# Kernel tuning notes

Hardware: AMD Instinct MI355X
Metric: run time of the kernel (lower is better)

## Reference

```python
import jax, jax.numpy as jnp
import numpy as np

NBINS = 256  # skimage threshold_otsu default
RGB_W = jnp.array([0.2989, 0.5870, 0.1140], dtype=jnp.float32)  # tf.image.rgb_to_grayscale weights


def threshold_otsu(img):
    """Global Otsu threshold over all pixels, matching skimage.filters.threshold_otsu."""
    vmin = img.min()
    vmax = img.max()
    edges = jnp.linspace(vmin, vmax, NBINS + 1)
    centers = (edges[:-1] + edges[1:]) * 0.5
    hist = jnp.histogram(img.ravel(), bins=edges)[0].astype(jnp.float32)
    # class probabilities / cumulative weights
    w1 = jnp.cumsum(hist)                      # weight of class <= t
    w2 = jnp.cumsum(hist[::-1])[::-1]          # weight of class > t
    hc = hist * centers
    s1 = jnp.cumsum(hc)
    s2 = jnp.cumsum(hc[::-1])[::-1]
    m1 = s1 / jnp.maximum(w1, 1.0)
    m2 = s2 / jnp.maximum(w2, 1.0)
    # inter-class variance at each split point
    var12 = w1[:-1] * w2[1:] * (m1[:-1] - m2[1:]) ** 2
    idx = jnp.argmax(var12)
    return centers[idx]


def setup_inputs() -> dict:
    key = jax.random.key(0)
    inputs = jax.random.uniform(key, (32, 128, 2048, 3), dtype=jnp.float32)
    return {"inputs": inputs}


def reference(inputs) -> jnp.ndarray:
    # rgb_to_grayscale on first 3 channels, keep channel dim -> [B,H,W,1]
    gray = jnp.einsum('bhwc,c->bhw', inputs[..., :3].astype(jnp.float32), RGB_W)[..., None]
    thresh = threshold_otsu(gray)
    binarized = (gray > thresh).astype(jnp.float32)   # [B,H,W,1]
    # channels == 3 -> tile grayscale binarization back to 3 channels
    binarized = jnp.tile(binarized, (1, 1, 1, 3))
    return binarized
```

## Files before the change

### kernel.cpp

```cpp
#include <hip/hip_runtime.h>

static constexpr int HIST_OFF   = 2;
static constexpr int EDGES_OFF  = 258;
static constexpr int VMIN_OFF   = 515;
static constexpr int DELTA_OFF  = 516;
static constexpr int INVD_OFF   = 517;
static constexpr int THRESH_OFF = 518;
static constexpr size_t GRAY_BYTE_OFF = 4096;

typedef float nfloat4 __attribute__((ext_vector_type(4)));

#define GLOAD_LDS16(gp, lp)                                                    \
    __builtin_amdgcn_global_load_lds(                                          \
        (const __attribute__((address_space(1))) void*)(gp),                   \
        (__attribute__((address_space(3))) void*)(lp), 16, 0, 0)

__device__ __forceinline__ unsigned fkey(float x) {
    unsigned u = __float_as_uint(x);
    return (u & 0x80000000u) ? ~u : (u | 0x80000000u);
}
__device__ __forceinline__ float keyf(unsigned k) {
    return (k & 0x80000000u) ? __uint_as_float(k & 0x7FFFFFFFu)
                             : __uint_as_float(~k);
}
__device__ __forceinline__ float gray1(float r, float g, float b) {
    float t0 = __fmul_rn(r, 0.2989f);
    float t1 = __fmul_rn(g, 0.5870f);
    float t2 = __fmul_rn(b, 0.1140f);
    return __fadd_rn(__fadd_rn(t0, t1), t2);
}

__global__ void init_kernel(unsigned* __restrict__ wsu) {
    int i = threadIdx.x;
    if (i < 256) wsu[HIST_OFF + i] = 0u;
    if (i == 0) { wsu[0] = 0xFFFFFFFFu; wsu[1] = 0u; }
}

__global__ void __launch_bounds__(256)
gray_minmax_async(const float* __restrict__ in, float* __restrict__ gray,
                  unsigned* __restrict__ wsu, int npix4) {
    __shared__ float4 sbuf[4][2][192];
    __shared__ unsigned smn[4], smx[4];
    const float4* in4 = (const float4*)in;
    float4* gray4 = (float4*)gray;
    const int lane = threadIdx.x & 63;
    const int w = threadIdx.x >> 6;
    const int gw = blockIdx.x * 4 + w;
    const size_t wbase4 = (size_t)gw * 768;
    unsigned mn = 0xFFFFFFFFu, mx = 0u;

#pragma unroll
    for (int k = 0; k < 3; ++k)
        GLOAD_LDS16(in4 + wbase4 + 64 * k + lane, &sbuf[w][0][64 * k]);

#pragma unroll
    for (int t = 0; t < 4; ++t) {
        const int cb = t & 1;
        if (t < 3) {
#pragma unroll
            for (int k = 0; k < 3; ++k)
                GLOAD_LDS16(in4 + wbase4 + (size_t)(t + 1) * 192 + 64 * k + lane,
                            &sbuf[w][cb ^ 1][64 * k]);
            __builtin_amdgcn_s_waitcnt(0x0F73);
        } else {
            __builtin_amdgcn_s_waitcnt(0x0F71);
        }
        float4 c0 = sbuf[w][cb][3 * lane + 0];
        float4 c1 = sbuf[w][cb][3 * lane + 1];
        float4 c2 = sbuf[w][cb][3 * lane + 2];
        float g0 = gray1(c0.x, c0.y, c0.z);
        float g1 = gray1(c0.w, c1.x, c1.y);
        float g2 = gray1(c1.z, c1.w, c2.x);
        float g3 = gray1(c2.y, c2.z, c2.w);
        gray4[(size_t)gw * 256 + t * 64 + lane] = make_float4(g0, g1, g2, g3);
        unsigned k0 = fkey(g0), k1 = fkey(g1), k2 = fkey(g2), k3 = fkey(g3);
        mn = min(mn, min(min(k0, k1), min(k2, k3)));
        mx = max(mx, max(max(k0, k1), max(k2, k3)));
    }
    for (int off = 32; off > 0; off >>= 1) {
        mn = min(mn, (unsigned)__shfl_xor((int)mn, off, 64));
        mx = max(mx, (unsigned)__shfl_xor((int)mx, off, 64));
    }
    if (lane == 0) { smn[w] = mn; smx[w] = mx; }
    __syncthreads();
    if (threadIdx.x == 0) {
        mn = min(min(smn[0], smn[1]), min(smn[2], smn[3]));
        mx = max(max(smx[0], smx[1]), max(smx[2], smx[3]));
        atomicMin(&wsu[0], mn);
        atomicMax(&wsu[1], mx);
    }
}

__global__ void __launch_bounds__(256)
gray_minmax_generic(const float* __restrict__ in, float* __restrict__ gray,
                    unsigned* __restrict__ wsu, int npix4) {
    __shared__ unsigned smn[4], smx[4];
    const float4* in4 = (const float4*)in;
    const int stride = gridDim.x * blockDim.x;
    unsigned mn = 0xFFFFFFFFu, mx = 0u;
    for (int t = blockIdx.x * blockDim.x + threadIdx.x; t < npix4; t += stride) {
        const float4* p = in4 + (size_t)t * 3;
        float4 c0 = p[0], c1 = p[1], c2 = p[2];
        float g0 = gray1(c0.x, c0.y, c0.z);
        float g1 = gray1(c0.w, c1.x, c1.y);
        float g2 = gray1(c1.z, c1.w, c2.x);
        float g3 = gray1(c2.y, c2.z, c2.w);
        if (gray) ((float4*)gray)[t] = make_float4(g0, g1, g2, g3);
        unsigned k0 = fkey(g0), k1 = fkey(g1), k2 = fkey(g2), k3 = fkey(g3);
        mn = min(mn, min(min(k0, k1), min(k2, k3)));
        mx = max(mx, max(max(k0, k1), max(k2, k3)));
    }
    for (int off = 32; off > 0; off >>= 1) {
        mn = min(mn, (unsigned)__shfl_xor((int)mn, off, 64));
        mx = max(mx, (unsigned)__shfl_xor((int)mx, off, 64));
    }
    int wave = threadIdx.x >> 6;
    if ((threadIdx.x & 63) == 0) { smn[wave] = mn; smx[wave] = mx; }
    __syncthreads();
    if (threadIdx.x == 0) {
        mn = min(min(smn[0], smn[1]), min(smn[2], smn[3]));
        mx = max(max(smx[0], smx[1]), max(smx[2], smx[3]));
        atomicMin(&wsu[0], mn);
        atomicMax(&wsu[1], mx);
    }
}

__global__ void edges_kernel(const unsigned* __restrict__ wsu,
                             float* __restrict__ wsf) {
    float vmin = keyf(wsu[0]);
    float vmax = keyf(wsu[1]);
    float delta = __fdiv_rn(__fsub_rn(vmax, vmin), 256.0f);
    int i = threadIdx.x;
    if (i <= 256) {
        float e = (i == 256) ? vmax
                             : __fadd_rn(vmin, __fmul_rn((float)i, delta));
        wsf[EDGES_OFF + i] = e;
    }
    if (i == 0) {
        wsf[VMIN_OFF]  = vmin;
        wsf[DELTA_OFF] = delta;
        wsf[INVD_OFF]  = (delta > 0.0f) ? __fdiv_rn(1.0f, delta) : 0.0f;
    }
}

__device__ __forceinline__ void bin4(float x0, float x1, float x2, float x3,
                                     const float* eds, float vmin, float invd,
                                     unsigned* lh) {
    float xs[4] = {x0, x1, x2, x3};
#pragma unroll
    for (int j = 0; j < 4; ++j) {
        float x = xs[j];
        int b = (int)(__fmul_rn(__fsub_rn(x, vmin), invd));
        b = b < 0 ? 0 : (b > 255 ? 255 : b);
        while (b < 255 && x >= eds[b + 1]) ++b;
        while (b > 0 && x < eds[b]) --b;
        atomicAdd(&lh[b], 1u);
    }
}

__global__ void __launch_bounds__(256)
hist_kernel(const float* __restrict__ gray, const float* __restrict__ in,
            const float* __restrict__ wsf, unsigned* __restrict__ wsu,
            int npix4) {
    __shared__ float eds[257];
    __shared__ unsigned lh[256];
    for (int i = threadIdx.x; i < 257; i += blockDim.x)
        eds[i] = wsf[EDGES_OFF + i];
    if (threadIdx.x < 256) lh[threadIdx.x] = 0u;
    __syncthreads();
    const float vmin = eds[0];
    const float invd = wsf[INVD_OFF];
    const int stride = gridDim.x * blockDim.x;
    const int base = blockIdx.x * blockDim.x + threadIdx.x;
    if (gray && base + 7 * stride < npix4) {
        float4 g[8];
#pragma unroll
        for (int j = 0; j < 8; ++j) g[j] = ((const float4*)gray)[base + j * stride];
#pragma unroll
        for (int j = 0; j < 8; ++j)
            bin4(g[j].x, g[j].y, g[j].z, g[j].w, eds, vmin, invd, lh);
    } else {
        for (int t = base; t < npix4; t += stride) {
            float4 g4;
            if (gray) g4 = ((const float4*)gray)[t];
            else {
                const float4* p = (const float4*)in + (size_t)t * 3;
                float4 c0 = p[0], c1 = p[1], c2 = p[2];
                g4 = make_float4(gray1(c0.x, c0.y, c0.z), gray1(c0.w, c1.x, c1.y),
                                 gray1(c1.z, c1.w, c2.x), gray1(c2.y, c2.z, c2.w));
            }
            bin4(g4.x, g4.y, g4.z, g4.w, eds, vmin, invd, lh);
        }
    }
    __syncthreads();
    if (threadIdx.x < 256 && lh[threadIdx.x] != 0u)
        atomicAdd(&wsu[HIST_OFF + threadIdx.x], lh[threadIdx.x]);
}

__global__ void otsu_kernel(const unsigned* __restrict__ wsu,
                            float* __restrict__ wsf) {
    __shared__ float histf[256];
    __shared__ float centers[256];
    __shared__ float w2a[256];
    __shared__ float s2a[256];
    int i = threadIdx.x;
    float e0 = wsf[EDGES_OFF + i];
    float e1 = wsf[EDGES_OFF + i + 1];
    centers[i] = __fmul_rn(__fadd_rn(e0, e1), 0.5f);
    histf[i] = (float)wsu[HIST_OFF + i];
    __syncthreads();
    if (i == 0) {
        float w = 0.0f, s = 0.0f;
        for (int t = 255; t >= 0; --t) {
            w = __fadd_rn(w, histf[t]);
            s = __fadd_rn(s, __fmul_rn(histf[t], centers[t]));
            w2a[t] = w;
            s2a[t] = s;
        }
        float w1 = 0.0f, s1 = 0.0f, best = -1.0f;
        int bidx = 0;
        for (int t = 0; t < 255; ++t) {
            w1 = __fadd_rn(w1, histf[t]);
            s1 = __fadd_rn(s1, __fmul_rn(histf[t], centers[t]));
            float m1 = __fdiv_rn(s1, fmaxf(w1, 1.0f));
            float m2 = __fdiv_rn(s2a[t + 1], fmaxf(w2a[t + 1], 1.0f));
            float d  = __fsub_rn(m1, m2);
            float v  = __fmul_rn(__fmul_rn(w1, w2a[t + 1]), __fmul_rn(d, d));
            if (v > best) { best = v; bidx = t; }
        }
        wsf[THRESH_OFF] = centers[bidx];
    }
}

__global__ void __launch_bounds__(256)
binarize_fast(const float* __restrict__ gray, const float* __restrict__ wsf,
              float* __restrict__ out, int npix4) {
    const float thr = wsf[THRESH_OFF];
    const nfloat4* gray4 = (const nfloat4*)gray;
    nfloat4* out4 = (nfloat4*)out;
    const int lane = threadIdx.x & 63;
    const int gw = (blockIdx.x * blockDim.x + threadIdx.x) >> 6;
    const int ma = lane / 3,         qa = lane % 3;
    const int mb = (64 + lane) / 3,  qb = (64 + lane) % 3;
    const int mc = (128 + lane) / 3, qc = (128 + lane) % 3;

    nfloat4 g[4];
    bool full[4];
#pragma unroll
    for (int r = 0; r < 4; ++r) {
        int gbase = gw * 256 + r * 64;
        full[r] = (gbase + 64 <= npix4);
        if (full[r]) g[r] = gray4[gbase + lane];
    }
#pragma unroll
    for (int r = 0; r < 4; ++r) {
        const int gbase = gw * 256 + r * 64;
        if (full[r]) {
            unsigned u = (g[r].x > thr ? 1u : 0u) |
                         (g[r].y > thr ? 0x100u : 0u) |
                         (g[r].z > thr ? 0x10000u : 0u) |
                         (g[r].w > thr ? 0x1000000u : 0u);
            const int rb = 3 * gbase;
#pragma unroll
            for (int k = 0; k < 3; ++k) {
                int m = (k == 0) ? ma : (k == 1) ? mb : mc;
                int q = (k == 0) ? qa : (k == 1) ? qb : qc;
                unsigned w = (unsigned)__builtin_amdgcn_ds_bpermute(4 * m,
                                                                    (int)u);
                float h0 = (w & 0xffu)       ? 1.0f : 0.0f;
                float h1 = (w & 0xff00u)     ? 1.0f : 0.0f;
                float h2 = (w & 0xff0000u)   ? 1.0f : 0.0f;
                float h3 = (w & 0xff000000u) ? 1.0f : 0.0f;
                nfloat4 o;
                o.x = (q == 0) ? h0 : (q == 1) ? h1 : h2;
                o.y = (q == 0) ? h0 : (q == 1) ? h1 : h3;
                o.z = (q == 0) ? h0 : (q == 1) ? h2 : h3;
                o.w = (q == 0) ? h1 : (q == 1) ? h2 : h3;
                __builtin_nontemporal_store(o, &out4[rb + 64 * k + lane]);
            }
        } else {
            int t = gbase + lane;
            if (t < npix4) {
                nfloat4 gg = gray4[t];
                float b0 = (gg.x > thr) ? 1.0f : 0.0f;
                float b1 = (gg.y > thr) ? 1.0f : 0.0f;
                float b2 = (gg.z > thr) ? 1.0f : 0.0f;
                float b3 = (gg.w > thr) ? 1.0f : 0.0f;
                nfloat4* o = out4 + (size_t)t * 3;
                __builtin_nontemporal_store((nfloat4){b0, b0, b0, b1}, &o[0]);
                __builtin_nontemporal_store((nfloat4){b1, b1, b2, b2}, &o[1]);
                __builtin_nontemporal_store((nfloat4){b2, b3, b3, b3}, &o[2]);
            }
        }
    }
}

__global__ void __launch_bounds__(256)
binarize_generic(const float* __restrict__ gray, const float* __restrict__ in,
                 const float* __restrict__ wsf, float* __restrict__ out,
                 int npix4) {
    const float thr = wsf[THRESH_OFF];
    const int stride = gridDim.x * blockDim.x;
    nfloat4* out4 = (nfloat4*)out;
    for (int t = blockIdx.x * blockDim.x + threadIdx.x; t < npix4; t += stride) {
        float4 g4;
        if (gray) g4 = ((const float4*)gray)[t];
        else {
            const float4* p = (const float4*)in + (size_t)t * 3;
            float4 c0 = p[0], c1 = p[1], c2 = p[2];
            g4 = make_float4(gray1(c0.x, c0.y, c0.z), gray1(c0.w, c1.x, c1.y),
                             gray1(c1.z, c1.w, c2.x), gray1(c2.y, c2.z, c2.w));
        }
        float b0 = (g4.x > thr) ? 1.0f : 0.0f;
        float b1 = (g4.y > thr) ? 1.0f : 0.0f;
        float b2 = (g4.z > thr) ? 1.0f : 0.0f;
        float b3 = (g4.w > thr) ? 1.0f : 0.0f;
        nfloat4* o = out4 + (size_t)t * 3;
        o[0] = (nfloat4){b0, b0, b0, b1};
        o[1] = (nfloat4){b1, b1, b2, b2};
        o[2] = (nfloat4){b2, b3, b3, b3};
    }
}

extern "C" void kernel_launch(void* const* d_in, const int* in_sizes, int n_in,
                              void* d_out, int out_size, void* d_ws,
                              size_t ws_size, hipStream_t stream) {
    const float* in = (const float*)d_in[0];
    float* out = (float*)d_out;
    int npix  = out_size / 3;
    int npix4 = npix / 4;
    unsigned* wsu = (unsigned*)d_ws;
    float* wsf = (float*)d_ws;
    size_t need = GRAY_BYTE_OFF + (size_t)npix * sizeof(float);
    float* gray = (ws_size >= need)
                      ? (float*)((char*)d_ws + GRAY_BYTE_OFF)
                      : nullptr;

    hipLaunchKernelGGL(init_kernel, dim3(1), dim3(256), 0, stream, wsu);
    if (gray && npix4 % 1024 == 0) {
        hipLaunchKernelGGL(gray_minmax_async, dim3(npix4 / 1024), dim3(256), 0,
                           stream, in, gray, wsu, npix4);
    } else {
        hipLaunchKernelGGL(gray_minmax_generic, dim3(2048), dim3(256), 0,
                           stream, in, gray, wsu, npix4);
    }
    hipLaunchKernelGGL(edges_kernel, dim3(1), dim3(320), 0, stream, wsu, wsf);
    hipLaunchKernelGGL(hist_kernel, dim3(1024), dim3(256), 0, stream,
                       gray, in, wsf, wsu, npix4);
    hipLaunchKernelGGL(otsu_kernel, dim3(1), dim3(256), 0, stream, wsu, wsf);
    if (gray) {
        hipLaunchKernelGGL(binarize_fast, dim3((npix4 + 1023) / 1024),
                           dim3(256), 0, stream, gray, wsf, out, npix4);
    } else {
        hipLaunchKernelGGL(binarize_generic, dim3(2048), dim3(256), 0, stream,
                           gray, in, wsf, out, npix4);
    }
}
```

Measured before the change: 282.2 us.

## Fold edges and Otsu kernels into histogram and binarize kernels

Removes the single-block edges_kernel and otsu_kernel launches. Each histogram block now recomputes the bin edges from the min/max keys, and each binarize block redundantly recomputes the histogram scan and Otsu threshold in shared memory after prefetching its gray values. This cuts two serial tiny launches from the pipeline. In exchange, every binarize block does a serial 256-step scan on one thread, and the fallback path for a missing gray workspace is dropped.

New measurement: 318.1 us. 12.7% more time.

```diff
diff --git a/kernel.cpp b/kernel.cpp
--- a/kernel.cpp
+++ b/kernel.cpp
@@ -1,11 +1,6 @@
 #include <hip/hip_runtime.h>
 
-static constexpr int HIST_OFF   = 2;
-static constexpr int EDGES_OFF  = 258;
-static constexpr int VMIN_OFF   = 515;
-static constexpr int DELTA_OFF  = 516;
-static constexpr int INVD_OFF   = 517;
-static constexpr int THRESH_OFF = 518;
+static constexpr int HIST_OFF = 2;
 static constexpr size_t GRAY_BYTE_OFF = 4096;
 
 typedef float nfloat4 __attribute__((ext_vector_type(4)));
@@ -28,6 +23,41 @@
     float t1 = __fmul_rn(g, 0.5870f);
     float t2 = __fmul_rn(b, 0.1140f);
     return __fadd_rn(__fadd_rn(t0, t1), t2);
+}
+__device__ __forceinline__ unsigned aload(const unsigned* p) {
+    return __hip_atomic_load(p, __ATOMIC_RELAXED, __HIP_MEMORY_SCOPE_AGENT);
+}
+
+__device__ __forceinline__ void build_edges(float* eds, float vmin, float vmax,
+                                            float delta) {
+    if (threadIdx.x < 256)
+        eds[threadIdx.x] =
+            __fadd_rn(vmin, __fmul_rn((float)threadIdx.x, delta));
+    if (threadIdx.x == 0) eds[256] = vmax;
+}
+
+__device__ __forceinline__ float otsu_scan(const float* histf,
+                                           const float* centers, float* w2a,
+                                           float* s2a) {
+    float w = 0.0f, s = 0.0f;
+    for (int t = 255; t >= 0; --t) {
+        w = __fadd_rn(w, histf[t]);
+        s = __fadd_rn(s, __fmul_rn(histf[t], centers[t]));
+        w2a[t] = w;
+        s2a[t] = s;
+    }
+    float w1 = 0.0f, s1 = 0.0f, best = -1.0f;
+    int bidx = 0;
+    for (int t = 0; t < 255; ++t) {
+        w1 = __fadd_rn(w1, histf[t]);
+        s1 = __fadd_rn(s1, __fmul_rn(histf[t], centers[t]));
+        float m1 = __fdiv_rn(s1, fmaxf(w1, 1.0f));
+        float m2 = __fdiv_rn(s2a[t + 1], fmaxf(w2a[t + 1], 1.0f));
+        float d  = __fsub_rn(m1, m2);
+        float v  = __fmul_rn(__fmul_rn(w1, w2a[t + 1]), __fmul_rn(d, d));
+        if (v > best) { best = v; bidx = t; }
+    }
+    return centers[bidx];
 }
 
 __global__ void init_kernel(unsigned* __restrict__ wsu) {
@@ -105,7 +135,7 @@
         float g1 = gray1(c0.w, c1.x, c1.y);
         float g2 = gray1(c1.z, c1.w, c2.x);
         float g3 = gray1(c2.y, c2.z, c2.w);
-        if (gray) ((float4*)gray)[t] = make_float4(g0, g1, g2, g3);
+        ((float4*)gray)[t] = make_float4(g0, g1, g2, g3);
         unsigned k0 = fkey(g0), k1 = fkey(g1), k2 = fkey(g2), k3 = fkey(g3);
         mn = min(mn, min(min(k0, k1), min(k2, k3)));
         mx = max(mx, max(max(k0, k1), max(k2, k3)));
@@ -125,71 +155,55 @@
     }
 }
 
-__global__ void edges_kernel(const unsigned* __restrict__ wsu,
-                             float* __restrict__ wsf) {
-    float vmin = keyf(wsu[0]);
-    float vmax = keyf(wsu[1]);
-    float delta = __fdiv_rn(__fsub_rn(vmax, vmin), 256.0f);
-    int i = threadIdx.x;
-    if (i <= 256) {
-        float e = (i == 256) ? vmax
-                             : __fadd_rn(vmin, __fmul_rn((float)i, delta));
-        wsf[EDGES_OFF + i] = e;
-    }
-    if (i == 0) {
-        wsf[VMIN_OFF]  = vmin;
-        wsf[DELTA_OFF] = delta;
-        wsf[INVD_OFF]  = (delta > 0.0f) ? __fdiv_rn(1.0f, delta) : 0.0f;
-    }
-}
-
-__device__ __forceinline__ void bin4(float x0, float x1, float x2, float x3,
-                                     const float* eds, float vmin, float invd,
-                                     unsigned* lh) {
-    float xs[4] = {x0, x1, x2, x3};
-#pragma unroll
-    for (int j = 0; j < 4; ++j) {
-        float x = xs[j];
-        int b = (int)(__fmul_rn(__fsub_rn(x, vmin), invd));
-        b = b < 0 ? 0 : (b > 255 ? 255 : b);
-        while (b < 255 && x >= eds[b + 1]) ++b;
-        while (b > 0 && x < eds[b]) --b;
-        atomicAdd(&lh[b], 1u);
-    }
-}
-
 __global__ void __launch_bounds__(256)
-hist_kernel(const float* __restrict__ gray, const float* __restrict__ in,
-            const float* __restrict__ wsf, unsigned* __restrict__ wsu,
+hist_kernel(const float* __restrict__ gray, unsigned* __restrict__ wsu,
             int npix4) {
     __shared__ float eds[257];
     __shared__ unsigned lh[256];
-    for (int i = threadIdx.x; i < 257; i += blockDim.x)
-        eds[i] = wsf[EDGES_OFF + i];
+    __shared__ unsigned skey[2];
+    if (threadIdx.x == 0) { skey[0] = aload(&wsu[0]); skey[1] = aload(&wsu[1]); }
+    __syncthreads();
+    const float vmin = keyf(skey[0]);
+    const float vmax = keyf(skey[1]);
+    const float delta = __fdiv_rn(__fsub_rn(vmax, vmin), 256.0f);
+    const float invd = (delta > 0.0f) ? __fdiv_rn(1.0f, delta) : 0.0f;
+    build_edges(eds, vmin, vmax, delta);
     if (threadIdx.x < 256) lh[threadIdx.x] = 0u;
     __syncthreads();
-    const float vmin = eds[0];
-    const float invd = wsf[INVD_OFF];
+
     const int stride = gridDim.x * blockDim.x;
     const int base = blockIdx.x * blockDim.x + threadIdx.x;
-    if (gray && base + 7 * stride < npix4) {
+    if (base + 7 * stride < npix4) {
         float4 g[8];
 #pragma unroll
-        for (int j = 0; j < 8; ++j) g[j] = ((const float4*)gray)[base + j * stride];
-#pragma unroll
         for (int j = 0; j < 8; ++j)
-            bin4(g[j].x, g[j].y, g[j].z, g[j].w, eds, vmin, invd, lh);
+            g[j] = ((const float4*)gray)[base + j * stride];
+#pragma unroll
+        for (int j = 0; j < 8; ++j) {
+            float xs[4] = {g[j].x, g[j].y, g[j].z, g[j].w};
+#pragma unroll
+            for (int i = 0; i < 4; ++i) {
+                float x = xs[i];
+                int b = (int)(__fmul_rn(__fsub_rn(x, vmin), invd));
+                b = b < 0 ? 0 : (b > 255 ? 255 : b);
+                while (b < 255 && x >= eds[b + 1]) ++b;
+                while (b > 0 && x < eds[b]) --b;
+                atomicAdd(&lh[b], 1u);
+            }
+        }
     } else {
         for (int t = base; t < npix4; t += stride) {
-            float4 g4;
-            if (gray) g4 = ((const float4*)gray)[t];
-            else {
-                const float4* p = (const float4*)in + (size_t)t * 3;
-                float4 c0 = p[0], c1 = p[1], c2 = p[2];
-                g4 = make_float4(gray1(c0.x, c0.y, c0.z), gray1(c0.w, c1.x, c1.y),
-                                 gray1(c1.z, c1.w, c2.x), gray1(c2.y, c2.z, c2.w));
-            }
-            bin4(g4.x, g4.y, g4.z, g4.w, eds, vmin, invd, lh);
+            float4 g4 = ((const float4*)gray)[t];
+            float xs[4] = {g4.x, g4.y, g4.z, g4.w};
+#pragma unroll
+            for (int i = 0; i < 4; ++i) {
+                float x = xs[i];
+                int b = (int)(__fmul_rn(__fsub_rn(x, vmin), invd));
+                b = b < 0 ? 0 : (b > 255 ? 255 : b);
+                while (b < 255 && x >= eds[b + 1]) ++b;
+                while (b > 0 && x < eds[b]) --b;
+                atomicAdd(&lh[b], 1u);
+            }
         }
     }
     __syncthreads();
@@ -197,45 +211,12 @@
         atomicAdd(&wsu[HIST_OFF + threadIdx.x], lh[threadIdx.x]);
 }
 
-__global__ void otsu_kernel(const unsigned* __restrict__ wsu,
-                            float* __restrict__ wsf) {
-    __shared__ float histf[256];
-    __shared__ float centers[256];
-    __shared__ float w2a[256];
-    __shared__ float s2a[256];
-    int i = threadIdx.x;
-    float e0 = wsf[EDGES_OFF + i];
-    float e1 = wsf[EDGES_OFF + i + 1];
-    centers[i] = __fmul_rn(__fadd_rn(e0, e1), 0.5f);
-    histf[i] = (float)wsu[HIST_OFF + i];
-    __syncthreads();
-    if (i == 0) {
-        float w = 0.0f, s = 0.0f;
-        for (int t = 255; t >= 0; --t) {
-            w = __fadd_rn(w, histf[t]);
-            s = __fadd_rn(s, __fmul_rn(histf[t], centers[t]));
-            w2a[t] = w;
-            s2a[t] = s;
-        }
-        float w1 = 0.0f, s1 = 0.0f, best = -1.0f;
-        int bidx = 0;
-        for (int t = 0; t < 255; ++t) {
-            w1 = __fadd_rn(w1, histf[t]);
-            s1 = __fadd_rn(s1, __fmul_rn(histf[t], centers[t]));
-            float m1 = __fdiv_rn(s1, fmaxf(w1, 1.0f));
-            float m2 = __fdiv_rn(s2a[t + 1], fmaxf(w2a[t + 1], 1.0f));
-            float d  = __fsub_rn(m1, m2);
-            float v  = __fmul_rn(__fmul_rn(w1, w2a[t + 1]), __fmul_rn(d, d));
-            if (v > best) { best = v; bidx = t; }
-        }
-        wsf[THRESH_OFF] = centers[bidx];
-    }
-}
-
 __global__ void __launch_bounds__(256)
-binarize_fast(const float* __restrict__ gray, const float* __restrict__ wsf,
+binarize_fast(const float* __restrict__ gray, const unsigned* __restrict__ wsu,
               float* __restrict__ out, int npix4) {
-    const float thr = wsf[THRESH_OFF];
+    __shared__ float eds[257], histf[256], centers[256], w2a[256], s2a[256];
+    __shared__ unsigned skey[2];
+    __shared__ float sthr;
     const nfloat4* gray4 = (const nfloat4*)gray;
     nfloat4* out4 = (nfloat4*)out;
     const int lane = threadIdx.x & 63;
@@ -251,7 +232,34 @@
         int gbase = gw * 256 + r * 64;
         full[r] = (gbase + 64 <= npix4);
         if (full[r]) g[r] = gray4[gbase + lane];
-    }
+        else {
+            int t = gbase + lane;
+            if (t < npix4) {
+                g[r].x = gray[(size_t)t * 4 + 0];
+                g[r].y = gray[(size_t)t * 4 + 1];
+                g[r].z = gray[(size_t)t * 4 + 2];
+                g[r].w = gray[(size_t)t * 4 + 3];
+            }
+        }
+    }
+
+    if (threadIdx.x == 0) { skey[0] = aload(&wsu[0]); skey[1] = aload(&wsu[1]); }
+    __syncthreads();
+    const float vmin = keyf(skey[0]);
+    const float vmax = keyf(skey[1]);
+    const float delta = __fdiv_rn(__fsub_rn(vmax, vmin), 256.0f);
+    build_edges(eds, vmin, vmax, delta);
+    if (threadIdx.x < 256)
+        histf[threadIdx.x] = (float)aload(&wsu[HIST_OFF + threadIdx.x]);
+    __syncthreads();
+    if (threadIdx.x < 256)
+        centers[threadIdx.x] =
+            __fmul_rn(__fadd_rn(eds[threadIdx.x], eds[threadIdx.x + 1]), 0.5f);
+    __syncthreads();
+    if (threadIdx.x == 0) sthr = otsu_scan(histf, centers, w2a, s2a);
+    __syncthreads();
+    const float thr = sthr;
+
 #pragma unroll
     for (int r = 0; r < 4; ++r) {
         const int gbase = gw * 256 + r * 64;
@@ -281,44 +289,16 @@
         } else {
             int t = gbase + lane;
             if (t < npix4) {
-                nfloat4 gg = gray4[t];
-                float b0 = (gg.x > thr) ? 1.0f : 0.0f;
-                float b1 = (gg.y > thr) ? 1.0f : 0.0f;
-                float b2 = (gg.z > thr) ? 1.0f : 0.0f;
-                float b3 = (gg.w > thr) ? 1.0f : 0.0f;
+                float b0 = (g[r].x > thr) ? 1.0f : 0.0f;
+                float b1 = (g[r].y > thr) ? 1.0f : 0.0f;
+                float b2 = (g[r].z > thr) ? 1.0f : 0.0f;
+                float b3 = (g[r].w > thr) ? 1.0f : 0.0f;
                 nfloat4* o = out4 + (size_t)t * 3;
                 __builtin_nontemporal_store((nfloat4){b0, b0, b0, b1}, &o[0]);
                 __builtin_nontemporal_store((nfloat4){b1, b1, b2, b2}, &o[1]);
                 __builtin_nontemporal_store((nfloat4){b2, b3, b3, b3}, &o[2]);
             }
         }
-    }
-}
-
-__global__ void __launch_bounds__(256)
-binarize_generic(const float* __restrict__ gray, const float* __restrict__ in,
-                 const float* __restrict__ wsf, float* __restrict__ out,
-                 int npix4) {
-    const float thr = wsf[THRESH_OFF];
-    const int stride = gridDim.x * blockDim.x;
-    nfloat4* out4 = (nfloat4*)out;
-    for (int t = blockIdx.x * blockDim.x + threadIdx.x; t < npix4; t += stride) {
-        float4 g4;
-        if (gray) g4 = ((const float4*)gray)[t];
-        else {
-            const float4* p = (const float4*)in + (size_t)t * 3;
-            float4 c0 = p[0], c1 = p[1], c2 = p[2];
-            g4 = make_float4(gray1(c0.x, c0.y, c0.z), gray1(c0.w, c1.x, c1.y),
-                             gray1(c1.z, c1.w, c2.x), gray1(c2.y, c2.z, c2.w));
-        }
-        float b0 = (g4.x > thr) ? 1.0f : 0.0f;
-        float b1 = (g4.y > thr) ? 1.0f : 0.0f;
-        float b2 = (g4.z > thr) ? 1.0f : 0.0f;
-        float b3 = (g4.w > thr) ? 1.0f : 0.0f;
-        nfloat4* o = out4 + (size_t)t * 3;
-        o[0] = (nfloat4){b0, b0, b0, b1};
-        o[1] = (nfloat4){b1, b1, b2, b2};
-        o[2] = (nfloat4){b2, b3, b3, b3};
     }
 }
 
@@ -330,29 +310,18 @@
     int npix  = out_size / 3;
     int npix4 = npix / 4;
     unsigned* wsu = (unsigned*)d_ws;
-    float* wsf = (float*)d_ws;
-    size_t need = GRAY_BYTE_OFF + (size_t)npix * sizeof(float);
-    float* gray = (ws_size >= need)
-                      ? (float*)((char*)d_ws + GRAY_BYTE_OFF)
-                      : nullptr;
+    float* gray = (float*)((char*)d_ws + GRAY_BYTE_OFF);
 
     hipLaunchKernelGGL(init_kernel, dim3(1), dim3(256), 0, stream, wsu);
-    if (gray && npix4 % 1024 == 0) {
+    if (npix4 % 1024 == 0) {
         hipLaunchKernelGGL(gray_minmax_async, dim3(npix4 / 1024), dim3(256), 0,
                            stream, in, gray, wsu, npix4);
     } else {
         hipLaunchKernelGGL(gray_minmax_generic, dim3(2048), dim3(256), 0,
                            stream, in, gray, wsu, npix4);
     }
-    hipLaunchKernelGGL(edges_kernel, dim3(1), dim3(320), 0, stream, wsu, wsf);
     hipLaunchKernelGGL(hist_kernel, dim3(1024), dim3(256), 0, stream,
-                       gray, in, wsf, wsu, npix4);
-    hipLaunchKernelGGL(otsu_kernel, dim3(1), dim3(256), 0, stream, wsu, wsf);
-    if (gray) {
-        hipLaunchKernelGGL(binarize_fast, dim3((npix4 + 1023) / 1024),
-                           dim3(256), 0, stream, gray, wsf, out, npix4);
-    } else {
-        hipLaunchKernelGGL(binarize_generic, dim3(2048), dim3(256), 0, stream,
-                           gray, in, wsf, out, npix4);
-    }
-}
+                       gray, wsu, npix4);
+    hipLaunchKernelGGL(binarize_fast, dim3((npix4 + 1023) / 1024), dim3(256),
+                       0, stream, gray, wsu, out, npix4);
+}
```
